# Kernel tuning notes

Measured on AMD Instinct MI355X. Metric: run time of the kernel, lower is better.

Reference implementation:

```python
import jax, jax.numpy as jnp
import numpy as np

T, B, OBS, H, A = 256, 128, 512, 1024, 18


def setup_inputs() -> dict:
    key = jax.random.key(0)
    ks = jax.random.split(key, 9)
    s = 0.02
    return {
        "state": jax.random.normal(ks[0], (T, B, OBS), dtype=jnp.float32),
        "mask": jax.random.randint(ks[1], (T, B), 0, 2, dtype=jnp.int32),
        "W_enc": jax.random.normal(ks[2], (H, OBS), dtype=jnp.float32) * s,
        "b_enc": jnp.zeros((H,), dtype=jnp.float32),
        "W_ih": jax.random.normal(ks[3], (4 * H, H), dtype=jnp.float32) * s,
        "W_hh": jax.random.normal(ks[4], (4 * H, H), dtype=jnp.float32) * s,
        "b_ih": jnp.zeros((4 * H,), dtype=jnp.float32),
        "b_hh": jnp.zeros((4 * H,), dtype=jnp.float32),
        "W_dec": jax.random.normal(ks[5], (A, H), dtype=jnp.float32) * s,
        "b_dec": jnp.zeros((A,), dtype=jnp.float32),
    }


def reference(state, mask, W_enc, b_enc, W_ih, W_hh, b_ih, b_hh, W_dec, b_dec):
    maskf = mask.astype(state.dtype)  # (T, B)
    hidden = W_hh.shape[1]
    # encode all timesteps in one GEMM: (T,B,OBS) @ (OBS,H)
    encoded = jax.nn.relu(jnp.einsum('tbo,ho->tbh', state, W_enc) + b_enc)
    # precompute input contribution to all gates (T,B,4H)
    x_gates = jnp.einsum('tbh,gh->tbg', encoded, W_ih) + b_ih + b_hh
    h0 = jnp.zeros((state.shape[1], hidden), dtype=state.dtype)
    c0 = jnp.zeros_like(h0)

    def step(carry, inp):
        h, c = carry
        xg, m = inp  # xg: (B,4H), m: (B,)
        gates = xg + h @ W_hh.T
        i, f, g, o = jnp.split(gates, 4, axis=-1)  # PyTorch LSTMCell gate order
        i = jax.nn.sigmoid(i)
        f = jax.nn.sigmoid(f)
        g = jnp.tanh(g)
        o = jax.nn.sigmoid(o)
        c_new = (f * c + i * g) * m[:, None]
        h_new = (o * jnp.tanh(f * c + i * g)) * m[:, None]
        return (h_new, c_new), h_new

    (h, c), latent = jax.lax.scan(step, (h0, c0), (x_gates, maskf))
    # decode all timesteps in one GEMM, then apply mask
    values = jnp.einsum('tbh,ah->tba', latent, W_dec) + b_dec
    values = values * maskf[:, :, None]
    return values, h, c
```

## Files before the change

### kernel.cpp

```cpp
#include <hip/hip_runtime.h>

#define T_STEPS 256
#define BATCH   128
#define OBSD    512
#define HID     1024
#define GH      4096
#define ACTD    18
#define TBROWS  (T_STEPS*BATCH)
#define NWG     256
#define JG      16

typedef __bf16 bf16x8_t __attribute__((ext_vector_type(8)));
typedef float  f32x4_t  __attribute__((ext_vector_type(4)));

__device__ __forceinline__ ushort f2bf(float f) {
  unsigned u = __builtin_bit_cast(unsigned, f);
  u += 0x7fffu + ((u >> 16) & 1u);
  return (ushort)(u >> 16);
}
__device__ __forceinline__ float bf2f(ushort s) {
  return __builtin_bit_cast(float, ((unsigned)s) << 16);
}
__device__ __forceinline__ f32x4_t mfma16(bf16x8_t a, bf16x8_t b, f32x4_t c) {
  return __builtin_amdgcn_mfma_f32_16x16x32_bf16(a, b, c, 0, 0, 0);
}
__device__ __forceinline__ void gl_lds16(const void* g, void* l) {
  __builtin_amdgcn_global_load_lds(
      (__attribute__((address_space(1))) void*)(g),
      (__attribute__((address_space(3))) void*)(l), 16, 0, 0);
}
__device__ __forceinline__ float sigm(float x) { return 1.f / (1.f + __expf(-x)); }
__device__ __forceinline__ float tanhf_fast(float x) {
  float e = __expf(2.f * x);
  return (e - 1.f) / (e + 1.f);
}
#define WAITVM(N) __builtin_amdgcn_s_waitcnt(0x0F70 | ((N) & 15))
__device__ __forceinline__ void wait_vm0() { __builtin_amdgcn_s_waitcnt(0x0F70); }

__global__ void cast_bf16_kernel(const float* __restrict__ in, ushort* __restrict__ out, int n4) {
  int i = blockIdx.x * blockDim.x + threadIdx.x;
  int stride = gridDim.x * blockDim.x;
  for (; i < n4; i += stride) {
    float4 v = reinterpret_cast<const float4*>(in)[i];
    ushort4 o;
    o.x = f2bf(v.x); o.y = f2bf(v.y); o.z = f2bf(v.z); o.w = f2bf(v.w);
    reinterpret_cast<ushort4*>(out)[i] = o;
  }
}

__global__ void cast_permute_wih_kernel(const float* __restrict__ in, ushort* __restrict__ out) {
  int idx = blockIdx.x * 256 + threadIdx.x;
  int rowd = idx >> 7;
  int c8 = (idx & 127) << 3;
  int g = rowd & 3, hid = rowd >> 2;
  const float* src = in + ((size_t)g * HID + hid) * HID + c8;
  ushort* dst = out + (size_t)rowd * HID + c8;
#pragma unroll
  for (int i = 0; i < 8; ++i) dst[i] = f2bf(src[i]);
}

__global__ void bias_perm_kernel(const float* __restrict__ bih, const float* __restrict__ bhh,
                                 float* __restrict__ out) {
  int i = blockIdx.x * 256 + threadIdx.x;
  int g = i & 3, hid = i >> 2;
  out[i] = bih[g * HID + hid] + bhh[g * HID + hid];
}

__global__ __launch_bounds__(256) void gemm_bt_kernel(
    const ushort* __restrict__ A, const ushort* __restrict__ Bt,
    const float* __restrict__ bias1,
    ushort* __restrict__ C, int M, int N, int K, int relu,
    const int* __restrict__ omask, float* __restrict__ ovals)
{
  __shared__ ushort la[128 * 64];
  __shared__ ushort lb[128 * 64];

  const int tid  = threadIdx.x;
  const int lane = tid & 63;
  const int w    = tid >> 6;
  const int wm   = w >> 1, wn = w & 1;
  const int nwg = gridDim.x;
  const int q8  = nwg >> 3;
  const int bid = (blockIdx.x & 7) * q8 + (blockIdx.x >> 3);
  const int ntiles = N >> 7;
  const int bm = bid / ntiles, bn = bid % ntiles;
  const size_t m0 = (size_t)bm << 7, n0 = (size_t)bn << 7;

  const int lrow = lane & 15;
  const int lk   = (lane >> 4) << 3;
  const int wavebase = (tid & ~63);

  f32x4_t acc[4][4];
  const f32x4_t zero = {0.f, 0.f, 0.f, 0.f};
#pragma unroll
  for (int i = 0; i < 4; ++i)
#pragma unroll
    for (int j = 0; j < 4; ++j) acc[i][j] = zero;

  for (int k0 = 0; k0 < K; k0 += 64) {
#pragma unroll
    for (int p = 0; p < 4; ++p) {
      int c = p * 256 + tid;
      int r = c >> 3;
      int q = (c & 7) << 3;
      gl_lds16(A + (m0 + r) * (size_t)K + k0 + q, la + (size_t)(p * 256 + wavebase) * 8);
      gl_lds16(Bt + (n0 + r) * (size_t)K + k0 + q, lb + (size_t)(p * 256 + wavebase) * 8);
    }
    __syncthreads();
#pragma unroll
    for (int kk = 0; kk < 64; kk += 32) {
      bf16x8_t af[4], bfr[4];
#pragma unroll
      for (int i = 0; i < 4; ++i)
        af[i] = *(const bf16x8_t*)(la + (wm * 64 + i * 16 + lrow) * 64 + kk + lk);
#pragma unroll
      for (int j = 0; j < 4; ++j)
        bfr[j] = *(const bf16x8_t*)(lb + (wn * 64 + j * 16 + lrow) * 64 + kk + lk);
#pragma unroll
      for (int i = 0; i < 4; ++i)
#pragma unroll
        for (int j = 0; j < 4; ++j)
          acc[i][j] = mfma16(af[i], bfr[j], acc[i][j]);
    }
    __syncthreads();
  }

  const int crow0 = (lane >> 4) * 4;
  if (ovals) {
#pragma unroll
    for (int j = 0; j < 4; ++j) {
      int col = wn * 64 + j * 16 + lrow;
      if (col < ACTD) {
        float bv = bias1[col];
#pragma unroll
        for (int i = 0; i < 4; ++i) {
#pragma unroll
          for (int r = 0; r < 4; ++r) {
            size_t row = m0 + wm * 64 + i * 16 + crow0 + r;
            float mv = (float)omask[row];
            ovals[row * ACTD + col] = (acc[i][j][r] + bv) * mv;
          }
        }
      }
    }
    return;
  }
#pragma unroll
  for (int j = 0; j < 4; ++j) {
    int col = (int)n0 + wn * 64 + j * 16 + lrow;
    float bv = bias1 ? bias1[col] : 0.f;
#pragma unroll
    for (int i = 0; i < 4; ++i) {
#pragma unroll
      for (int r = 0; r < 4; ++r) {
        size_t row = m0 + wm * 64 + i * 16 + crow0 + r;
        float v = acc[i][j][r] + bv;
        if (relu) v = fmaxf(v, 0.f);
        C[row * (size_t)N + col] = f2bf(v);
      }
    }
  }
}

__global__ __launch_bounds__(512, 2) void gemm256_kernel(
    const ushort* __restrict__ A, const ushort* __restrict__ Bt,
    const float* __restrict__ bias,
    ushort* __restrict__ C, int M, int N, int K, int relu)
{
  __shared__ __align__(16) ushort lds[2][2][16384];

  const int tid  = threadIdx.x;
  const int lane = tid & 63;
  const int wid  = tid >> 6;
  const int wm   = wid >> 2, wn = wid & 3;
  const int nwg  = gridDim.x;
  const int q8   = nwg >> 3;
  const int bid  = (blockIdx.x & 7) * q8 + (blockIdx.x >> 3);
  const int ntiles = N >> 8;
  const int bm = bid / ntiles, bn = bid % ntiles;
  const size_t m0 = (size_t)bm << 8, n0 = (size_t)bn << 8;

  const int lrow = lane & 15;
  const int lkg  = lane >> 4;

  int srow[4], sgsr[4];
#pragma unroll
  for (int q = 0; q < 4; ++q) {
    int s = (q * 8 + wid) * 64 + lane;
    srow[q] = s >> 3;
    sgsr[q] = (s & 7) ^ ((s >> 3) & 7);
  }

#define STAGE256(BUF, KT) do {                                                \
    const size_t kb_ = (size_t)(KT) * 64;                                     \
    _Pragma("unroll")                                                         \
    for (int q = 0; q < 4; ++q) {                                             \
      gl_lds16(A  + (m0 + srow[q]) * (size_t)K + kb_ + sgsr[q] * 8,           \
               &lds[BUF][0][(q * 8 + wid) * 512]);                            \
      gl_lds16(Bt + (n0 + srow[q]) * (size_t)K + kb_ + sgsr[q] * 8,           \
               &lds[BUF][1][(q * 8 + wid) * 512]);                            \
    }                                                                         \
  } while (0)

  f32x4_t acc[8][4];
  const f32x4_t zero = {0.f, 0.f, 0.f, 0.f};
#pragma unroll
  for (int f = 0; f < 8; ++f)
#pragma unroll
    for (int n = 0; n < 4; ++n) acc[f][n] = zero;

  const int nkt = K >> 6;
  STAGE256(0, 0);
  STAGE256(1, 1);

  for (int kt = 0; kt < nkt; ++kt) {
    const int buf = kt & 1;
    if (kt + 1 < nkt) WAITVM(8); else WAITVM(0);
    __builtin_amdgcn_s_barrier();
    __builtin_amdgcn_sched_barrier(0);
#pragma unroll
    for (int p = 0; p < 4; ++p) {
      const int kk = p >> 1, mg = p & 1;
      bf16x8_t av[4], bv[4];
#pragma unroll
      for (int f = 0; f < 4; ++f) {
        int ar = wm * 128 + (mg * 4 + f) * 16 + lrow;
        int ags = (kk * 4 + lkg) ^ (ar & 7);
        av[f] = *(const bf16x8_t*)&lds[buf][0][ar * 64 + ags * 8];
      }
#pragma unroll
      for (int n = 0; n < 4; ++n) {
        int br = wn * 64 + n * 16 + lrow;
        int bgs = (kk * 4 + lkg) ^ (br & 7);
        bv[n] = *(const bf16x8_t*)&lds[buf][1][br * 64 + bgs * 8];
      }
      __builtin_amdgcn_s_setprio(1);
#pragma unroll
      for (int f = 0; f < 4; ++f)
#pragma unroll
        for (int n = 0; n < 4; ++n)
          acc[mg * 4 + f][n] = mfma16(av[f], bv[n], acc[mg * 4 + f][n]);
      __builtin_amdgcn_s_setprio(0);
    }
    __builtin_amdgcn_s_barrier();
    if (kt + 2 < nkt) STAGE256(buf, kt + 2);
  }
#undef STAGE256

  const int crow0 = lkg * 4;
#pragma unroll
  for (int n = 0; n < 4; ++n) {
    int col = (int)n0 + wn * 64 + n * 16 + lrow;
    float bvv = bias ? bias[col] : 0.f;
#pragma unroll
    for (int f = 0; f < 8; ++f) {
#pragma unroll
      for (int r = 0; r < 4; ++r) {
        size_t row = m0 + (size_t)wm * 128 + f * 16 + crow0 + r;
        float v = acc[f][n][r] + bvv;
        if (relu) v = fmaxf(v, 0.f);
        C[row * (size_t)N + col] = f2bf(v);
      }
    }
  }
}

__global__ __launch_bounds__(256, 1) void lstm_scan_kernel(
    const ushort* __restrict__ xg,
    const ushort* __restrict__ whh,
    const int* __restrict__ mask,
    const ushort* __restrict__ hinit,
    ushort* __restrict__ hseq,
    float* __restrict__ cbuf,
    float* __restrict__ outh, float* __restrict__ outc,
    unsigned* __restrict__ flags,
    int t0, int nsteps)
{
  __shared__ __align__(16) ushort lds_pool[64 * 1024];
  __shared__ __align__(16) ushort hexch[32 * 16];

  const int tid  = threadIdx.x;
  const int lane = tid & 63;
  const int w    = tid >> 6;
  const int wg   = blockIdx.x;
  const int bq   = wg >> 6;
  const int jg   = wg & 63;
  const int j0   = jg * JG;
  const int b0   = bq * 32;

  const int lrow = lane & 15;
  const int lkg  = lane >> 4;

  for (int c = tid; c < 64 * 128; c += 256) {
    int r = c >> 7, gn = c & 127;
    int jj = r >> 2, g = r & 3;
    const ushort* src = whh + ((size_t)g * HID + j0 + jj) * HID + gn * 8;
    int gnd = (gn & ~7) | ((gn & 7) ^ (r & 7));
    *reinterpret_cast<uint4*>(&lds_pool[r * 1024 + gnd * 8]) =
        *reinterpret_cast<const uint4*>(src);
  }
  __syncthreads();

  bf16x8_t af[8][4];
#pragma unroll
  for (int kc = 0; kc < 8; ++kc) {
#pragma unroll
    for (int ks = 0; ks < 4; ++ks) {
      int gA = kc * 16 + ks * 4 + lkg;
      int gAs = (gA & ~7) | ((gA & 7) ^ (lrow & 7));
      af[kc][ks] = *(const bf16x8_t*)(lds_pool + (size_t)(w * 16 + lrow) * 1024 + gAs * 8);
    }
  }
  __syncthreads();
  ushort* hstg = lds_pool;

  const int jjc = w * 4 + lkg;
  const int bl0 = lrow, bl1 = 16 + lrow;

  float creg0, creg1;
  if (t0 == 0) { creg0 = creg1 = 0.f; }
  else {
    creg0 = cbuf[(size_t)(b0 + bl0) * HID + j0 + jjc];
    creg1 = cbuf[(size_t)(b0 + bl1) * HID + j0 + jjc];
  }

  const int s0 = w * 128 + lane;
  const int s1 = s0 + 64;
  const int sb0 = s0 >> 4, sq0 = s0 & 15;
  const int sb1 = s1 >> 4, sq1 = s1 & 15;
  const int gg0 = (sq0 & 8) | ((sq0 & 7) ^ (sb0 & 7));
  const int gg1 = (sq1 & 8) | ((sq1 & 7) ^ (sb1 & 7));

  const unsigned* fpoll = &flags[(size_t)(bq * 64 + lane) * 16];

  ushort4 xv0, xv1;
  float m0v, m1v;
  {
    xv0 = *(const ushort4*)(xg + (size_t)(b0 + bl0) * GH + (j0 + jjc) * 4);
    xv1 = *(const ushort4*)(xg + (size_t)(b0 + bl1) * GH + (j0 + jjc) * 4);
    m0v = (float)mask[b0 + bl0];
    m1v = (float)mask[b0 + bl1];
  }
  __builtin_amdgcn_sched_barrier(0);

#define CHUNK(KC, VN) do {                                                     \
    __builtin_amdgcn_s_waitcnt(0x0F70 | (VN));                                 \
    __builtin_amdgcn_s_barrier();                                              \
    __builtin_amdgcn_sched_barrier(0);                                         \
    const ushort* sbuf = hstg + (size_t)(KC) * 4096;                           \
    _Pragma("unroll")                                                          \
    for (int ks = 0; ks < 4; ++ks) {                                           \
      int q16 = ks * 4 + lkg;                                                  \
      int qs = (q16 & 8) | ((q16 & 7) ^ (bl0 & 7));                            \
      bf16x8_t bf0 = *(const bf16x8_t*)(sbuf + (size_t)bl0 * 128 + qs * 8);    \
      bf16x8_t bf1 = *(const bf16x8_t*)(sbuf + (size_t)bl1 * 128 + qs * 8);    \
      acc0 = mfma16(af[KC][ks], bf0, acc0);                                    \
      acc1 = mfma16(af[KC][ks], bf1, acc1);                                    \
    }                                                                          \
    __builtin_amdgcn_sched_barrier(0);                                         \
  } while (0)

  for (int tl = 0; tl < nsteps; ++tl) {
    const ushort* hsrc = (t0 + tl == 0)
        ? (hinit + (size_t)b0 * HID)
        : (hseq + (size_t)(t0 + tl - 1) * (BATCH * HID) + (size_t)b0 * HID);

    wait_vm0();
    __builtin_amdgcn_sched_barrier(0);

    f32x4_t acc0 = {0.f, 0.f, 0.f, 0.f};
    f32x4_t acc1 = {0.f, 0.f, 0.f, 0.f};

#pragma unroll
    for (int kc = 0; kc < 8; ++kc) {
      gl_lds16(hsrc + (size_t)sb0 * HID + (kc * 16 + gg0) * 8,
               hstg + (size_t)kc * 4096 + (size_t)(w * 128) * 8);
      gl_lds16(hsrc + (size_t)sb1 * HID + (kc * 16 + gg1) * 8,
               hstg + (size_t)kc * 4096 + (size_t)(w * 128 + 64) * 8);
    }
    __builtin_amdgcn_sched_barrier(0);

    CHUNK(0, 14); CHUNK(1, 12); CHUNK(2, 10); CHUNK(3, 8);
    CHUNK(4, 6);  CHUNK(5, 4);  CHUNK(6, 2);  CHUNK(7, 0);

    {
      float ig = sigm(acc0[0] + bf2f(xv0.x));
      float fg = sigm(acc0[1] + bf2f(xv0.y));
      float gt = tanhf_fast(acc0[2] + bf2f(xv0.z));
      float og = sigm(acc0[3] + bf2f(xv0.w));
      float cp = fg * creg0 + ig * gt;
      creg0 = cp * m0v;
      float h0 = og * tanhf_fast(cp) * m0v;

      ig = sigm(acc1[0] + bf2f(xv1.x));
      fg = sigm(acc1[1] + bf2f(xv1.y));
      gt = tanhf_fast(acc1[2] + bf2f(xv1.z));
      og = sigm(acc1[3] + bf2f(xv1.w));
      cp = fg * creg1 + ig * gt;
      creg1 = cp * m1v;
      float h1 = og * tanhf_fast(cp) * m1v;

      ushort hb0 = f2bf(h0), hb1 = f2bf(h1);
      hexch[bl0 * 16 + jjc] = hb0;
      hexch[bl1 * 16 + jjc] = hb1;
      if (t0 + tl == T_STEPS - 1) {
        outh[(size_t)(b0 + bl0) * HID + j0 + jjc] = h0;
        outh[(size_t)(b0 + bl1) * HID + j0 + jjc] = h1;
        outc[(size_t)(b0 + bl0) * HID + j0 + jjc] = creg0;
        outc[(size_t)(b0 + bl1) * HID + j0 + jjc] = creg1;
      }
    }
    __syncthreads();

    if (tid < 128) {
      int bl = tid >> 2, seg = tid & 3;
      unsigned long long v = *(const unsigned long long*)(&hexch[bl * 16 + seg * 4]);
      unsigned long long* dst = (unsigned long long*)(hseq +
          (size_t)(t0 + tl) * (BATCH * HID) + (size_t)(b0 + bl) * HID + j0 + seg * 4);
      __hip_atomic_store(dst, v, __ATOMIC_RELAXED, __HIP_MEMORY_SCOPE_AGENT);
    }

    if (tl != nsteps - 1) {
      __syncthreads();
      const unsigned tgt = (unsigned)(t0 + tl + 1);
      if (tid == 0)
        __hip_atomic_store(&flags[(size_t)wg * 16], tgt, __ATOMIC_RELAXED, __HIP_MEMORY_SCOPE_AGENT);
      {
        const ushort* xp = xg + (size_t)(tl + 1) * BATCH * GH;
        xv0 = *(const ushort4*)(xp + (size_t)(b0 + bl0) * GH + (j0 + jjc) * 4);
        xv1 = *(const ushort4*)(xp + (size_t)(b0 + bl1) * GH + (j0 + jjc) * 4);
        m0v = (float)mask[(tl + 1) * BATCH + b0 + bl0];
        m1v = (float)mask[(tl + 1) * BATCH + b0 + bl1];
      }
      __builtin_amdgcn_sched_barrier(0);
      if (tid < 64) {
        for (;;) {
          unsigned v = __hip_atomic_load(fpoll, __ATOMIC_RELAXED, __HIP_MEMORY_SCOPE_AGENT);
          if (__all(v >= tgt)) break;
        }
      }
      __syncthreads();
    }
  }
#undef CHUNK

  cbuf[(size_t)(b0 + bl0) * HID + j0 + jjc] = creg0;
  cbuf[(size_t)(b0 + bl1) * HID + j0 + jjc] = creg1;
}

extern "C" void kernel_launch(void* const* d_in, const int* in_sizes, int n_in,
                              void* d_out, int out_size, void* d_ws, size_t ws_size,
                              hipStream_t stream) {
  (void)in_sizes; (void)n_in; (void)out_size;
  const float* state = (const float*)d_in[0];
  const int*   mask  = (const int*)d_in[1];
  const float* Wenc  = (const float*)d_in[2];
  const float* benc  = (const float*)d_in[3];
  const float* Wih   = (const float*)d_in[4];
  const float* Whh   = (const float*)d_in[5];
  const float* bih   = (const float*)d_in[6];
  const float* bhh   = (const float*)d_in[7];
  const float* Wdec  = (const float*)d_in[8];
  const float* bdec  = (const float*)d_in[9];

  float* out_values = (float*)d_out;
  float* out_h = out_values + (size_t)TBROWS * ACTD;
  float* out_c = out_h + (size_t)BATCH * HID;

  auto pad256 = [](size_t b) { return (b + 255) & ~(size_t)255; };

  const size_t sz_wenc  = (size_t)HID * OBSD * 2;
  const size_t sz_wih   = (size_t)GH * HID * 2;
  const size_t sz_whh   = (size_t)GH * HID * 2;
  const size_t sz_wdec  = (size_t)128 * HID * 2;
  const size_t sz_bdec  = 512;
  const size_t sz_bperm = (size_t)GH * sizeof(float);
  const size_t sz_flags = NWG * 16 * sizeof(unsigned);
  const size_t sz_hseq  = (size_t)TBROWS * HID * 2;
  const size_t sz_hinit = (size_t)BATCH * HID * 2;
  const size_t sz_cbuf  = (size_t)BATCH * HID * 4;
  const size_t fixed = pad256(sz_wenc) + pad256(sz_wih) + pad256(sz_whh) +
                       pad256(sz_wdec) + pad256(sz_bdec) + pad256(sz_bperm) +
                       pad256(sz_flags) + pad256(sz_hseq) + pad256(sz_hinit) +
                       pad256(sz_cbuf);

  int Tc = 8;
  {
    const int cands[6] = {256, 128, 64, 32, 16, 8};
    for (int ci = 0; ci < 6; ++ci) {
      int tc = cands[ci];
      size_t per = pad256((size_t)tc * BATCH * HID * 2)
                 + pad256((size_t)tc * BATCH * GH * 2);
      if (fixed + per <= ws_size) { Tc = tc; break; }
    }
  }
  const int nchunks = T_STEPS / Tc;
  const int crows = Tc * BATCH;

  char* ws = (char*)d_ws;
  size_t off = 0;
  auto alloc = [&](size_t b) { char* r = ws + off; off += pad256(b); return r; };
  ushort* wenc_bf  = (ushort*)alloc(sz_wenc);
  ushort* wih_perm = (ushort*)alloc(sz_wih);
  ushort* whh_bf   = (ushort*)alloc(sz_whh);
  ushort* wdec_pad = (ushort*)alloc(sz_wdec);
  float*  bdec_pad = (float*)alloc(sz_bdec);
  float*  bperm    = (float*)alloc(sz_bperm);
  unsigned* flags  = (unsigned*)alloc(sz_flags);
  ushort* hseq     = (ushort*)alloc(sz_hseq);
  ushort* hinit    = (ushort*)alloc(sz_hinit);
  float*  cbuf     = (float*)alloc(sz_cbuf);
  ushort* enc_c    = (ushort*)alloc((size_t)crows * HID * 2);
  ushort* xg_c     = (ushort*)alloc((size_t)crows * GH * 2);
  ushort* state_c  = xg_c;

  hipMemsetAsync(hinit, 0, sz_hinit, stream);
  hipMemsetAsync(flags, 0, sz_flags, stream);
  hipMemsetAsync(wdec_pad, 0, sz_wdec, stream);
  hipMemsetAsync(bdec_pad, 0, sz_bdec, stream);
  hipMemcpyAsync(bdec_pad, bdec, ACTD * sizeof(float), hipMemcpyDeviceToDevice, stream);

  auto cast = [&](const float* src, ushort* dst, size_t n) {
    int n4 = (int)(n / 4);
    int blocks = (n4 + 255) / 256;
    if (blocks > 4096) blocks = 4096;
    cast_bf16_kernel<<<blocks, 256, 0, stream>>>(src, dst, n4);
  };
  cast(Wenc, wenc_bf, (size_t)HID * OBSD);
  cast(Whh, whh_bf, (size_t)GH * HID);
  cast(Wdec, wdec_pad, (size_t)ACTD * HID);
  cast_permute_wih_kernel<<<(GH * 128) / 256, 256, 0, stream>>>(Wih, wih_perm);
  bias_perm_kernel<<<GH / 256, 256, 0, stream>>>(bih, bhh, bperm);

  for (int c = 0; c < nchunks; ++c) {
    const int t0 = c * Tc;
    cast(state + (size_t)t0 * BATCH * OBSD, state_c, (size_t)crows * OBSD);
    gemm256_kernel<<<(crows / 256) * (HID / 256), 512, 0, stream>>>(
        state_c, wenc_bf, benc, enc_c, crows, HID, OBSD, 1);
    gemm256_kernel<<<(crows / 256) * (GH / 256), 512, 0, stream>>>(
        enc_c, wih_perm, bperm, xg_c, crows, GH, HID, 0);
    lstm_scan_kernel<<<NWG, 256, 0, stream>>>(
        xg_c, whh_bf, mask + (size_t)t0 * BATCH, hinit, hseq, cbuf,
        out_h, out_c, flags, t0, Tc);
  }

  gemm_bt_kernel<<<TBROWS / 128, 256, 0, stream>>>(
      hseq, wdec_pad, bdec_pad, nullptr, TBROWS, 128, HID, 0,
      mask, out_values);
}
```

Measured before the change: 1.417 ms.

## Split LSTM scan batch into two half-tiles with per-wave flags to overlap sync

Each workgroup now handles two 16-row batch groups (A and B) drawn from different halves of the batch, not one 32-row group. B's recurrent matmul and gate math run while other workgroups are still consuming A's published h. Completion is signalled per wave through finer-grained flags, with a poll of four flags per lane at the start of each step instead of a whole-workgroup barrier plus a single flag. The goal is to hide inter-workgroup synchronisation latency on the serial recurrence. The cost is more flag traffic, more polling loads and less MFMA batching per chunk.

```diff
diff --git a/kernel.cpp b/kernel.cpp
--- a/kernel.cpp
+++ b/kernel.cpp
@@ -35,7 +35,8 @@
   return (e - 1.f) / (e + 1.f);
 }
 #define WAITVM(N) __builtin_amdgcn_s_waitcnt(0x0F70 | ((N) & 15))
-__device__ __forceinline__ void wait_vm0() { __builtin_amdgcn_s_waitcnt(0x0F70); }
+__device__ __forceinline__ void wait_vm0()   { __builtin_amdgcn_s_waitcnt(0x0F70); }
+__device__ __forceinline__ void wait_lgkm0() { __builtin_amdgcn_s_waitcnt(0xC07F); }
 
 __global__ void cast_bf16_kernel(const float* __restrict__ in, ushort* __restrict__ out, int n4) {
   int i = blockIdx.x * blockDim.x + threadIdx.x;
@@ -277,16 +278,19 @@
     int t0, int nsteps)
 {
   __shared__ __align__(16) ushort lds_pool[64 * 1024];
-  __shared__ __align__(16) ushort hexch[32 * 16];
+  __shared__ __align__(16) ushort hexA[4 * 64];
+  __shared__ __align__(16) ushort hexB[4 * 64];
 
   const int tid  = threadIdx.x;
   const int lane = tid & 63;
   const int w    = tid >> 6;
   const int wg   = blockIdx.x;
-  const int bq   = wg >> 6;
+  const int pg   = wg >> 6;
   const int jg   = wg & 63;
   const int j0   = jg * JG;
-  const int b0   = bq * 32;
+  const int b0A  = pg * 16;
+  const int b0B  = 64 + pg * 16;
+  const int eA   = pg, eB = pg + 4;
 
   const int lrow = lane & 15;
   const int lkg  = lane >> 4;
@@ -312,140 +316,174 @@
     }
   }
   __syncthreads();
-  ushort* hstg = lds_pool;
+  ushort* bufA = lds_pool;
+  ushort* bufB = lds_pool + 16384;
 
   const int jjc = w * 4 + lkg;
-  const int bl0 = lrow, bl1 = 16 + lrow;
-
-  float creg0, creg1;
-  if (t0 == 0) { creg0 = creg1 = 0.f; }
+  const int bl0 = lrow;
+
+  float cregA, cregB;
+  if (t0 == 0) { cregA = cregB = 0.f; }
   else {
-    creg0 = cbuf[(size_t)(b0 + bl0) * HID + j0 + jjc];
-    creg1 = cbuf[(size_t)(b0 + bl1) * HID + j0 + jjc];
-  }
-
-  const int s0 = w * 128 + lane;
-  const int s1 = s0 + 64;
-  const int sb0 = s0 >> 4, sq0 = s0 & 15;
-  const int sb1 = s1 >> 4, sq1 = s1 & 15;
-  const int gg0 = (sq0 & 8) | ((sq0 & 7) ^ (sb0 & 7));
-  const int gg1 = (sq1 & 8) | ((sq1 & 7) ^ (sb1 & 7));
-
-  const unsigned* fpoll = &flags[(size_t)(bq * 64 + lane) * 16];
-
-  ushort4 xv0, xv1;
-  float m0v, m1v;
+    cregA = cbuf[(size_t)(b0A + bl0) * HID + j0 + jjc];
+    cregB = cbuf[(size_t)(b0B + bl0) * HID + j0 + jjc];
+  }
+
+  const int sb = w * 4 + (lane >> 4);
+  const int sq = lane & 15;
+  const int gg = (sq & 8) | ((sq & 7) ^ (sb & 7));
+
+  unsigned* mfA = flags + ((size_t)(eA * 64 + jg) * 4 + w) * 16;
+  unsigned* mfB = flags + ((size_t)(eB * 64 + jg) * 4 + w) * 16;
+  const unsigned* fpA = flags + (size_t)(eA * 64 + lane) * 64;
+  const unsigned* fpB = flags + (size_t)(eB * 64 + lane) * 64;
+
+  ushort4 xvA, xvB;
+  float mA, mB;
   {
-    xv0 = *(const ushort4*)(xg + (size_t)(b0 + bl0) * GH + (j0 + jjc) * 4);
-    xv1 = *(const ushort4*)(xg + (size_t)(b0 + bl1) * GH + (j0 + jjc) * 4);
-    m0v = (float)mask[b0 + bl0];
-    m1v = (float)mask[b0 + bl1];
+    xvA = *(const ushort4*)(xg + (size_t)(b0A + bl0) * GH + (j0 + jjc) * 4);
+    xvB = *(const ushort4*)(xg + (size_t)(b0B + bl0) * GH + (j0 + jjc) * 4);
+    mA = (float)mask[b0A + bl0];
+    mB = (float)mask[b0B + bl0];
   }
   __builtin_amdgcn_sched_barrier(0);
 
-#define CHUNK(KC, VN) do {                                                     \
-    __builtin_amdgcn_s_waitcnt(0x0F70 | (VN));                                 \
+#define POLL4(FB, TGT) do {                                                       \
+    for (;;) {                                                                    \
+      unsigned v0 = __hip_atomic_load((FB),      __ATOMIC_RELAXED, __HIP_MEMORY_SCOPE_AGENT); \
+      unsigned v1 = __hip_atomic_load((FB) + 16, __ATOMIC_RELAXED, __HIP_MEMORY_SCOPE_AGENT); \
+      unsigned v2 = __hip_atomic_load((FB) + 32, __ATOMIC_RELAXED, __HIP_MEMORY_SCOPE_AGENT); \
+      unsigned v3 = __hip_atomic_load((FB) + 48, __ATOMIC_RELAXED, __HIP_MEMORY_SCOPE_AGENT); \
+      if (__all(v0 >= (TGT) && v1 >= (TGT) && v2 >= (TGT) && v3 >= (TGT))) break; \
+    }                                                                             \
+  } while (0)
+
+#define CHUNKA(KC) do {                                                        \
+    WAITVM(15 - (KC));                                                         \
     __builtin_amdgcn_s_barrier();                                              \
     __builtin_amdgcn_sched_barrier(0);                                         \
-    const ushort* sbuf = hstg + (size_t)(KC) * 4096;                           \
+    const ushort* sb_ = bufA + (size_t)(KC) * 2048;                            \
     _Pragma("unroll")                                                          \
     for (int ks = 0; ks < 4; ++ks) {                                           \
       int q16 = ks * 4 + lkg;                                                  \
       int qs = (q16 & 8) | ((q16 & 7) ^ (bl0 & 7));                            \
-      bf16x8_t bf0 = *(const bf16x8_t*)(sbuf + (size_t)bl0 * 128 + qs * 8);    \
-      bf16x8_t bf1 = *(const bf16x8_t*)(sbuf + (size_t)bl1 * 128 + qs * 8);    \
-      acc0 = mfma16(af[KC][ks], bf0, acc0);                                    \
-      acc1 = mfma16(af[KC][ks], bf1, acc1);                                    \
+      bf16x8_t bv = *(const bf16x8_t*)(sb_ + (size_t)bl0 * 128 + qs * 8);      \
+      accA = mfma16(af[KC][ks], bv, accA);                                     \
     }                                                                          \
     __builtin_amdgcn_sched_barrier(0);                                         \
   } while (0)
 
   for (int tl = 0; tl < nsteps; ++tl) {
-    const ushort* hsrc = (t0 + tl == 0)
-        ? (hinit + (size_t)b0 * HID)
-        : (hseq + (size_t)(t0 + tl - 1) * (BATCH * HID) + (size_t)b0 * HID);
-
+    const int gs = t0 + tl;
+    const ushort* hsA = (gs == 0)
+        ? (hinit + (size_t)b0A * HID)
+        : (hseq + (size_t)(gs - 1) * (BATCH * HID) + (size_t)b0A * HID);
+    const ushort* hsB = (gs == 0)
+        ? (hinit + (size_t)b0B * HID)
+        : (hseq + (size_t)(gs - 1) * (BATCH * HID) + (size_t)b0B * HID);
+    const unsigned tgt = (unsigned)gs;
+
+    POLL4(fpA, tgt);
+    POLL4(fpB, tgt);
+    __syncthreads();
+    __builtin_amdgcn_sched_barrier(0);
+
+    f32x4_t accA = {0.f, 0.f, 0.f, 0.f};
+    f32x4_t accB = {0.f, 0.f, 0.f, 0.f};
+
+#pragma unroll
+    for (int kc = 0; kc < 8; ++kc)
+      gl_lds16(hsA + (size_t)sb * HID + (kc * 16 + gg) * 8, bufA + (size_t)kc * 2048 + w * 512);
+#pragma unroll
+    for (int kc = 0; kc < 8; ++kc)
+      gl_lds16(hsB + (size_t)sb * HID + (kc * 16 + gg) * 8, bufB + (size_t)kc * 2048 + w * 512);
+    __builtin_amdgcn_sched_barrier(0);
+
+    CHUNKA(0); CHUNKA(1); CHUNKA(2); CHUNKA(3);
+    CHUNKA(4); CHUNKA(5); CHUNKA(6); CHUNKA(7);
+
+    {
+      float ig = sigm(accA[0] + bf2f(xvA.x));
+      float fg = sigm(accA[1] + bf2f(xvA.y));
+      float gt = tanhf_fast(accA[2] + bf2f(xvA.z));
+      float og = sigm(accA[3] + bf2f(xvA.w));
+      float cp = fg * cregA + ig * gt;
+      cregA = cp * mA;
+      float h = og * tanhf_fast(cp) * mA;
+      hexA[w * 64 + bl0 * 4 + lkg] = f2bf(h);
+      if (gs == T_STEPS - 1) {
+        outh[(size_t)(b0A + bl0) * HID + j0 + jjc] = h;
+        outc[(size_t)(b0A + bl0) * HID + j0 + jjc] = cregA;
+      }
+    }
+    wait_lgkm0();
+    __builtin_amdgcn_sched_barrier(0);
+    if (lane < 16) {
+      unsigned long long v = *(const unsigned long long*)(&hexA[w * 64 + lane * 4]);
+      __hip_atomic_store((unsigned long long*)(hseq + (size_t)gs * (BATCH * HID) +
+          (size_t)(b0A + lane) * HID + j0 + w * 4), v,
+          __ATOMIC_RELAXED, __HIP_MEMORY_SCOPE_AGENT);
+    }
     wait_vm0();
     __builtin_amdgcn_sched_barrier(0);
-
-    f32x4_t acc0 = {0.f, 0.f, 0.f, 0.f};
-    f32x4_t acc1 = {0.f, 0.f, 0.f, 0.f};
-
+    if (lane == 0)
+      __hip_atomic_store(mfA, (unsigned)(gs + 1), __ATOMIC_RELAXED, __HIP_MEMORY_SCOPE_AGENT);
+
+    __builtin_amdgcn_s_barrier();
+    __builtin_amdgcn_sched_barrier(0);
 #pragma unroll
     for (int kc = 0; kc < 8; ++kc) {
-      gl_lds16(hsrc + (size_t)sb0 * HID + (kc * 16 + gg0) * 8,
-               hstg + (size_t)kc * 4096 + (size_t)(w * 128) * 8);
-      gl_lds16(hsrc + (size_t)sb1 * HID + (kc * 16 + gg1) * 8,
-               hstg + (size_t)kc * 4096 + (size_t)(w * 128 + 64) * 8);
-    }
-    __builtin_amdgcn_sched_barrier(0);
-
-    CHUNK(0, 14); CHUNK(1, 12); CHUNK(2, 10); CHUNK(3, 8);
-    CHUNK(4, 6);  CHUNK(5, 4);  CHUNK(6, 2);  CHUNK(7, 0);
+#pragma unroll
+      for (int ks = 0; ks < 4; ++ks) {
+        int q16 = ks * 4 + lkg;
+        int qs = (q16 & 8) | ((q16 & 7) ^ (bl0 & 7));
+        bf16x8_t bv = *(const bf16x8_t*)(bufB + (size_t)kc * 2048 + (size_t)bl0 * 128 + qs * 8);
+        accB = mfma16(af[kc][ks], bv, accB);
+      }
+    }
+    __builtin_amdgcn_sched_barrier(0);
 
     {
-      float ig = sigm(acc0[0] + bf2f(xv0.x));
-      float fg = sigm(acc0[1] + bf2f(xv0.y));
-      float gt = tanhf_fast(acc0[2] + bf2f(xv0.z));
-      float og = sigm(acc0[3] + bf2f(xv0.w));
-      float cp = fg * creg0 + ig * gt;
-      creg0 = cp * m0v;
-      float h0 = og * tanhf_fast(cp) * m0v;
-
-      ig = sigm(acc1[0] + bf2f(xv1.x));
-      fg = sigm(acc1[1] + bf2f(xv1.y));
-      gt = tanhf_fast(acc1[2] + bf2f(xv1.z));
-      og = sigm(acc1[3] + bf2f(xv1.w));
-      cp = fg * creg1 + ig * gt;
-      creg1 = cp * m1v;
-      float h1 = og * tanhf_fast(cp) * m1v;
-
-      ushort hb0 = f2bf(h0), hb1 = f2bf(h1);
-      hexch[bl0 * 16 + jjc] = hb0;
-      hexch[bl1 * 16 + jjc] = hb1;
-      if (t0 + tl == T_STEPS - 1) {
-        outh[(size_t)(b0 + bl0) * HID + j0 + jjc] = h0;
-        outh[(size_t)(b0 + bl1) * HID + j0 + jjc] = h1;
-        outc[(size_t)(b0 + bl0) * HID + j0 + jjc] = creg0;
-        outc[(size_t)(b0 + bl1) * HID + j0 + jjc] = creg1;
-      }
-    }
-    __syncthreads();
-
-    if (tid < 128) {
-      int bl = tid >> 2, seg = tid & 3;
-      unsigned long long v = *(const unsigned long long*)(&hexch[bl * 16 + seg * 4]);
-      unsigned long long* dst = (unsigned long long*)(hseq +
-          (size_t)(t0 + tl) * (BATCH * HID) + (size_t)(b0 + bl) * HID + j0 + seg * 4);
-      __hip_atomic_store(dst, v, __ATOMIC_RELAXED, __HIP_MEMORY_SCOPE_AGENT);
-    }
-
-    if (tl != nsteps - 1) {
-      __syncthreads();
-      const unsigned tgt = (unsigned)(t0 + tl + 1);
-      if (tid == 0)
-        __hip_atomic_store(&flags[(size_t)wg * 16], tgt, __ATOMIC_RELAXED, __HIP_MEMORY_SCOPE_AGENT);
-      {
-        const ushort* xp = xg + (size_t)(tl + 1) * BATCH * GH;
-        xv0 = *(const ushort4*)(xp + (size_t)(b0 + bl0) * GH + (j0 + jjc) * 4);
-        xv1 = *(const ushort4*)(xp + (size_t)(b0 + bl1) * GH + (j0 + jjc) * 4);
-        m0v = (float)mask[(tl + 1) * BATCH + b0 + bl0];
-        m1v = (float)mask[(tl + 1) * BATCH + b0 + bl1];
-      }
-      __builtin_amdgcn_sched_barrier(0);
-      if (tid < 64) {
-        for (;;) {
-          unsigned v = __hip_atomic_load(fpoll, __ATOMIC_RELAXED, __HIP_MEMORY_SCOPE_AGENT);
-          if (__all(v >= tgt)) break;
-        }
-      }
-      __syncthreads();
-    }
-  }
-#undef CHUNK
-
-  cbuf[(size_t)(b0 + bl0) * HID + j0 + jjc] = creg0;
-  cbuf[(size_t)(b0 + bl1) * HID + j0 + jjc] = creg1;
+      float ig = sigm(accB[0] + bf2f(xvB.x));
+      float fg = sigm(accB[1] + bf2f(xvB.y));
+      float gt = tanhf_fast(accB[2] + bf2f(xvB.z));
+      float og = sigm(accB[3] + bf2f(xvB.w));
+      float cp = fg * cregB + ig * gt;
+      cregB = cp * mB;
+      float h = og * tanhf_fast(cp) * mB;
+      hexB[w * 64 + bl0 * 4 + lkg] = f2bf(h);
+      if (gs == T_STEPS - 1) {
+        outh[(size_t)(b0B + bl0) * HID + j0 + jjc] = h;
+        outc[(size_t)(b0B + bl0) * HID + j0 + jjc] = cregB;
+      }
+    }
+    wait_lgkm0();
+    __builtin_amdgcn_sched_barrier(0);
+    if (lane < 16) {
+      unsigned long long v = *(const unsigned long long*)(&hexB[w * 64 + lane * 4]);
+      __hip_atomic_store((unsigned long long*)(hseq + (size_t)gs * (BATCH * HID) +
+          (size_t)(b0B + lane) * HID + j0 + w * 4), v,
+          __ATOMIC_RELAXED, __HIP_MEMORY_SCOPE_AGENT);
+    }
+    wait_vm0();
+    __builtin_amdgcn_sched_barrier(0);
+    if (lane == 0)
+      __hip_atomic_store(mfB, (unsigned)(gs + 1), __ATOMIC_RELAXED, __HIP_MEMORY_SCOPE_AGENT);
+
+    if (tl + 1 < nsteps) {
+      const ushort* xp = xg + (size_t)(tl + 1) * BATCH * GH;
+      xvA = *(const ushort4*)(xp + (size_t)(b0A + bl0) * GH + (j0 + jjc) * 4);
+      xvB = *(const ushort4*)(xp + (size_t)(b0B + bl0) * GH + (j0 + jjc) * 4);
+      mA = (float)mask[(tl + 1) * BATCH + b0A + bl0];
+      mB = (float)mask[(tl + 1) * BATCH + b0B + bl0];
+    }
+    __builtin_amdgcn_sched_barrier(0);
+  }
+#undef CHUNKA
+#undef POLL4
+
+  cbuf[(size_t)(b0A + bl0) * HID + j0 + jjc] = cregA;
+  cbuf[(size_t)(b0B + bl0) * HID + j0 + jjc] = cregB;
 }
 
 extern "C" void kernel_launch(void* const* d_in, const int* in_sizes, int n_in,
@@ -475,7 +513,7 @@
   const size_t sz_wdec  = (size_t)128 * HID * 2;
   const size_t sz_bdec  = 512;
   const size_t sz_bperm = (size_t)GH * sizeof(float);
-  const size_t sz_flags = NWG * 16 * sizeof(unsigned);
+  const size_t sz_flags = (size_t)8 * 64 * 4 * 16 * sizeof(unsigned);
   const size_t sz_hseq  = (size_t)TBROWS * HID * 2;
   const size_t sz_hinit = (size_t)BATCH * HID * 2;
   const size_t sz_cbuf  = (size_t)BATCH * HID * 4;
```

Result: slower. 1.952 ms (+37.8%).

## Split LSTM scan over 512 workgroups with 16-row batch slices

Applied to the files above, without the earlier changes.

Each persistent scan workgroup now handles 16 batch rows instead of 32, so the grid doubles to 512 workgroups with launch bounds allowing two per CU. The W_hh slice staging goes through a smaller 32KB LDS pool in four passes so two workgroups fit per CU. The goal is to halve the per-step MFMA and activation work per workgroup and spread the recurrence over more CUs. In exchange each weight slice is loaded by twice as many workgroups, and the flag-based cross-workgroup synchronisation involves more participants and may co-reside two blocks per CU.

```diff
diff --git a/kernel.cpp b/kernel.cpp
--- a/kernel.cpp
+++ b/kernel.cpp
@@ -7,7 +7,7 @@
 #define GH      4096
 #define ACTD    18
 #define TBROWS  (T_STEPS*BATCH)
-#define NWG     256
+#define SNWG    512
 #define JG      16
 
 typedef __bf16 bf16x8_t __attribute__((ext_vector_type(8)));
@@ -265,7 +265,7 @@
   }
 }
 
-__global__ __launch_bounds__(256, 1) void lstm_scan_kernel(
+__global__ __launch_bounds__(256, 2) void lstm_scan_kernel(
     const ushort* __restrict__ xg,
     const ushort* __restrict__ whh,
     const int* __restrict__ mask,
@@ -276,161 +276,137 @@
     unsigned* __restrict__ flags,
     int t0, int nsteps)
 {
-  __shared__ __align__(16) ushort lds_pool[64 * 1024];
-  __shared__ __align__(16) ushort hexch[32 * 16];
+  __shared__ __align__(16) ushort pool[16 * 1024];
+  __shared__ __align__(16) ushort hexch[16 * 16];
 
   const int tid  = threadIdx.x;
   const int lane = tid & 63;
   const int w    = tid >> 6;
   const int wg   = blockIdx.x;
-  const int bq   = wg >> 6;
+  const int eg   = wg >> 6;
   const int jg   = wg & 63;
   const int j0   = jg * JG;
-  const int b0   = bq * 32;
+  const int b0   = eg * 16;
 
   const int lrow = lane & 15;
   const int lkg  = lane >> 4;
 
-  for (int c = tid; c < 64 * 128; c += 256) {
-    int r = c >> 7, gn = c & 127;
-    int jj = r >> 2, g = r & 3;
-    const ushort* src = whh + ((size_t)g * HID + j0 + jj) * HID + gn * 8;
-    int gnd = (gn & ~7) | ((gn & 7) ^ (r & 7));
-    *reinterpret_cast<uint4*>(&lds_pool[r * 1024 + gnd * 8]) =
-        *reinterpret_cast<const uint4*>(src);
-  }
-  __syncthreads();
-
   bf16x8_t af[8][4];
-#pragma unroll
-  for (int kc = 0; kc < 8; ++kc) {
-#pragma unroll
-    for (int ks = 0; ks < 4; ++ks) {
-      int gA = kc * 16 + ks * 4 + lkg;
-      int gAs = (gA & ~7) | ((gA & 7) ^ (lrow & 7));
-      af[kc][ks] = *(const bf16x8_t*)(lds_pool + (size_t)(w * 16 + lrow) * 1024 + gAs * 8);
-    }
-  }
-  __syncthreads();
-  ushort* hstg = lds_pool;
+#pragma unroll 1
+  for (int p = 0; p < 4; ++p) {
+    for (int c = tid; c < 16 * 128; c += 256) {
+      int rl = c >> 7, gn = c & 127;
+      int rr = p * 16 + rl;
+      int jj = rr >> 2, g = rr & 3;
+      const ushort* src = whh + ((size_t)g * HID + j0 + jj) * HID + gn * 8;
+      int gnd = (gn & ~7) | ((gn & 7) ^ (rl & 7));
+      *reinterpret_cast<uint4*>(&pool[rl * 1024 + gnd * 8]) =
+          *reinterpret_cast<const uint4*>(src);
+    }
+    __syncthreads();
+    if (w == p) {
+#pragma unroll
+      for (int kc = 0; kc < 8; ++kc)
+#pragma unroll
+        for (int ks = 0; ks < 4; ++ks) {
+          int gA = kc * 16 + ks * 4 + lkg;
+          int gAs = (gA & ~7) | ((gA & 7) ^ (lrow & 7));
+          af[kc][ks] = *(const bf16x8_t*)(pool + (size_t)lrow * 1024 + gAs * 8);
+        }
+    }
+    __syncthreads();
+  }
 
   const int jjc = w * 4 + lkg;
-  const int bl0 = lrow, bl1 = 16 + lrow;
-
-  float creg0, creg1;
-  if (t0 == 0) { creg0 = creg1 = 0.f; }
-  else {
-    creg0 = cbuf[(size_t)(b0 + bl0) * HID + j0 + jjc];
-    creg1 = cbuf[(size_t)(b0 + bl1) * HID + j0 + jjc];
-  }
-
-  const int s0 = w * 128 + lane;
-  const int s1 = s0 + 64;
-  const int sb0 = s0 >> 4, sq0 = s0 & 15;
-  const int sb1 = s1 >> 4, sq1 = s1 & 15;
-  const int gg0 = (sq0 & 8) | ((sq0 & 7) ^ (sb0 & 7));
-  const int gg1 = (sq1 & 8) | ((sq1 & 7) ^ (sb1 & 7));
-
-  const unsigned* fpoll = &flags[(size_t)(bq * 64 + lane) * 16];
-
-  ushort4 xv0, xv1;
-  float m0v, m1v;
+  const int bl0 = lrow;
+
+  float creg;
+  if (t0 == 0) creg = 0.f;
+  else creg = cbuf[(size_t)(b0 + bl0) * HID + j0 + jjc];
+
+  const int sb = w * 4 + (lane >> 4);
+  const int sq = lane & 15;
+  const int gg = (sq & 8) | ((sq & 7) ^ (sb & 7));
+
+  unsigned* myflag = flags + (size_t)(eg * 64 + jg) * 16;
+  const unsigned* fpoll = flags + (size_t)(eg * 64 + lane) * 16;
+
+  ushort4 xv;
+  float mv;
   {
-    xv0 = *(const ushort4*)(xg + (size_t)(b0 + bl0) * GH + (j0 + jjc) * 4);
-    xv1 = *(const ushort4*)(xg + (size_t)(b0 + bl1) * GH + (j0 + jjc) * 4);
-    m0v = (float)mask[b0 + bl0];
-    m1v = (float)mask[b0 + bl1];
+    xv = *(const ushort4*)(xg + (size_t)(b0 + bl0) * GH + (j0 + jjc) * 4);
+    mv = (float)mask[b0 + bl0];
   }
   __builtin_amdgcn_sched_barrier(0);
 
-#define CHUNK(KC, VN) do {                                                     \
-    __builtin_amdgcn_s_waitcnt(0x0F70 | (VN));                                 \
+#define CHUNK(KC) do {                                                         \
+    WAITVM(7 - (KC));                                                          \
     __builtin_amdgcn_s_barrier();                                              \
     __builtin_amdgcn_sched_barrier(0);                                         \
-    const ushort* sbuf = hstg + (size_t)(KC) * 4096;                           \
+    const ushort* sbuf = pool + (size_t)(KC) * 2048;                           \
     _Pragma("unroll")                                                          \
     for (int ks = 0; ks < 4; ++ks) {                                           \
       int q16 = ks * 4 + lkg;                                                  \
       int qs = (q16 & 8) | ((q16 & 7) ^ (bl0 & 7));                            \
-      bf16x8_t bf0 = *(const bf16x8_t*)(sbuf + (size_t)bl0 * 128 + qs * 8);    \
-      bf16x8_t bf1 = *(const bf16x8_t*)(sbuf + (size_t)bl1 * 128 + qs * 8);    \
-      acc0 = mfma16(af[KC][ks], bf0, acc0);                                    \
-      acc1 = mfma16(af[KC][ks], bf1, acc1);                                    \
+      bf16x8_t bv = *(const bf16x8_t*)(sbuf + (size_t)bl0 * 128 + qs * 8);     \
+      acc = mfma16(af[KC][ks], bv, acc);                                       \
     }                                                                          \
     __builtin_amdgcn_sched_barrier(0);                                         \
   } while (0)
 
   for (int tl = 0; tl < nsteps; ++tl) {
-    const ushort* hsrc = (t0 + tl == 0)
+    const int gs = t0 + tl;
+    const ushort* hsrc = (gs == 0)
         ? (hinit + (size_t)b0 * HID)
-        : (hseq + (size_t)(t0 + tl - 1) * (BATCH * HID) + (size_t)b0 * HID);
+        : (hseq + (size_t)(gs - 1) * (BATCH * HID) + (size_t)b0 * HID);
 
     wait_vm0();
     __builtin_amdgcn_sched_barrier(0);
 
-    f32x4_t acc0 = {0.f, 0.f, 0.f, 0.f};
-    f32x4_t acc1 = {0.f, 0.f, 0.f, 0.f};
-
-#pragma unroll
-    for (int kc = 0; kc < 8; ++kc) {
-      gl_lds16(hsrc + (size_t)sb0 * HID + (kc * 16 + gg0) * 8,
-               hstg + (size_t)kc * 4096 + (size_t)(w * 128) * 8);
-      gl_lds16(hsrc + (size_t)sb1 * HID + (kc * 16 + gg1) * 8,
-               hstg + (size_t)kc * 4096 + (size_t)(w * 128 + 64) * 8);
-    }
+    f32x4_t acc = {0.f, 0.f, 0.f, 0.f};
+
+#pragma unroll
+    for (int kc = 0; kc < 8; ++kc)
+      gl_lds16(hsrc + (size_t)sb * HID + (kc * 16 + gg) * 8,
+               pool + (size_t)kc * 2048 + (size_t)w * 512);
     __builtin_amdgcn_sched_barrier(0);
 
-    CHUNK(0, 14); CHUNK(1, 12); CHUNK(2, 10); CHUNK(3, 8);
-    CHUNK(4, 6);  CHUNK(5, 4);  CHUNK(6, 2);  CHUNK(7, 0);
+    CHUNK(0); CHUNK(1); CHUNK(2); CHUNK(3);
+    CHUNK(4); CHUNK(5); CHUNK(6); CHUNK(7);
 
     {
-      float ig = sigm(acc0[0] + bf2f(xv0.x));
-      float fg = sigm(acc0[1] + bf2f(xv0.y));
-      float gt = tanhf_fast(acc0[2] + bf2f(xv0.z));
-      float og = sigm(acc0[3] + bf2f(xv0.w));
-      float cp = fg * creg0 + ig * gt;
-      creg0 = cp * m0v;
-      float h0 = og * tanhf_fast(cp) * m0v;
-
-      ig = sigm(acc1[0] + bf2f(xv1.x));
-      fg = sigm(acc1[1] + bf2f(xv1.y));
-      gt = tanhf_fast(acc1[2] + bf2f(xv1.z));
-      og = sigm(acc1[3] + bf2f(xv1.w));
-      cp = fg * creg1 + ig * gt;
-      creg1 = cp * m1v;
-      float h1 = og * tanhf_fast(cp) * m1v;
-
-      ushort hb0 = f2bf(h0), hb1 = f2bf(h1);
-      hexch[bl0 * 16 + jjc] = hb0;
-      hexch[bl1 * 16 + jjc] = hb1;
-      if (t0 + tl == T_STEPS - 1) {
-        outh[(size_t)(b0 + bl0) * HID + j0 + jjc] = h0;
-        outh[(size_t)(b0 + bl1) * HID + j0 + jjc] = h1;
-        outc[(size_t)(b0 + bl0) * HID + j0 + jjc] = creg0;
-        outc[(size_t)(b0 + bl1) * HID + j0 + jjc] = creg1;
+      float ig = sigm(acc[0] + bf2f(xv.x));
+      float fg = sigm(acc[1] + bf2f(xv.y));
+      float gt = tanhf_fast(acc[2] + bf2f(xv.z));
+      float og = sigm(acc[3] + bf2f(xv.w));
+      float cp = fg * creg + ig * gt;
+      creg = cp * mv;
+      float h = og * tanhf_fast(cp) * mv;
+      hexch[bl0 * 16 + jjc] = f2bf(h);
+      if (gs == T_STEPS - 1) {
+        outh[(size_t)(b0 + bl0) * HID + j0 + jjc] = h;
+        outc[(size_t)(b0 + bl0) * HID + j0 + jjc] = creg;
       }
     }
     __syncthreads();
 
-    if (tid < 128) {
+    if (tid < 64) {
       int bl = tid >> 2, seg = tid & 3;
       unsigned long long v = *(const unsigned long long*)(&hexch[bl * 16 + seg * 4]);
       unsigned long long* dst = (unsigned long long*)(hseq +
-          (size_t)(t0 + tl) * (BATCH * HID) + (size_t)(b0 + bl) * HID + j0 + seg * 4);
+          (size_t)gs * (BATCH * HID) + (size_t)(b0 + bl) * HID + j0 + seg * 4);
       __hip_atomic_store(dst, v, __ATOMIC_RELAXED, __HIP_MEMORY_SCOPE_AGENT);
     }
 
     if (tl != nsteps - 1) {
       __syncthreads();
-      const unsigned tgt = (unsigned)(t0 + tl + 1);
+      const unsigned tgt = (unsigned)(gs + 1);
       if (tid == 0)
-        __hip_atomic_store(&flags[(size_t)wg * 16], tgt, __ATOMIC_RELAXED, __HIP_MEMORY_SCOPE_AGENT);
+        __hip_atomic_store(myflag, tgt, __ATOMIC_RELAXED, __HIP_MEMORY_SCOPE_AGENT);
       {
         const ushort* xp = xg + (size_t)(tl + 1) * BATCH * GH;
-        xv0 = *(const ushort4*)(xp + (size_t)(b0 + bl0) * GH + (j0 + jjc) * 4);
-        xv1 = *(const ushort4*)(xp + (size_t)(b0 + bl1) * GH + (j0 + jjc) * 4);
-        m0v = (float)mask[(tl + 1) * BATCH + b0 + bl0];
-        m1v = (float)mask[(tl + 1) * BATCH + b0 + bl1];
+        xv = *(const ushort4*)(xp + (size_t)(b0 + bl0) * GH + (j0 + jjc) * 4);
+        mv = (float)mask[(tl + 1) * BATCH + b0 + bl0];
       }
       __builtin_amdgcn_sched_barrier(0);
       if (tid < 64) {
@@ -444,8 +420,7 @@
   }
 #undef CHUNK
 
-  cbuf[(size_t)(b0 + bl0) * HID + j0 + jjc] = creg0;
-  cbuf[(size_t)(b0 + bl1) * HID + j0 + jjc] = creg1;
+  cbuf[(size_t)(b0 + bl0) * HID + j0 + jjc] = creg;
 }
 
 extern "C" void kernel_launch(void* const* d_in, const int* in_sizes, int n_in,
@@ -475,7 +450,7 @@
   const size_t sz_wdec  = (size_t)128 * HID * 2;
   const size_t sz_bdec  = 512;
   const size_t sz_bperm = (size_t)GH * sizeof(float);
-  const size_t sz_flags = NWG * 16 * sizeof(unsigned);
+  const size_t sz_flags = (size_t)SNWG * 16 * sizeof(unsigned);
   const size_t sz_hseq  = (size_t)TBROWS * HID * 2;
   const size_t sz_hinit = (size_t)BATCH * HID * 2;
   const size_t sz_cbuf  = (size_t)BATCH * HID * 4;
@@ -539,7 +514,7 @@
         state_c, wenc_bf, benc, enc_c, crows, HID, OBSD, 1);
     gemm256_kernel<<<(crows / 256) * (GH / 256), 512, 0, stream>>>(
         enc_c, wih_perm, bperm, xg_c, crows, GH, HID, 0);
-    lstm_scan_kernel<<<NWG, 256, 0, stream>>>(
+    lstm_scan_kernel<<<SNWG, 256, 0, stream>>>(
         xg_c, whh_bf, mask + (size_t)t0 * BATCH, hinit, hseq, cbuf,
         out_h, out_c, flags, t0, Tc);
   }
```

Result: faster. 1.297 ms (median of 2 runs) (-8.4%).
